# Performance work log

Hardware: AMD Instinct MI355X
Metric: run time of the kernel (lower is better)

The kernel has to match this reference:

```python
import jax, jax.numpy as jnp
import numpy as np

FEATURE_DIM = 128
EDGE_DIM = 32
N_NODES = 10000
BATCH = 4
N_EDGES = 640000
TEMPERATURE = 0.66
POWER_ITERS = 5


def spectral_normalize(W):
    # torch.nn.utils.spectral_norm: divide W by largest singular value estimated
    # via power iteration; u, v are treated as constants (no grad).
    # W: [out, in]
    u = jnp.ones((W.shape[0],), W.dtype) / jnp.sqrt(jnp.asarray(W.shape[0], W.dtype))
    for _ in range(POWER_ITERS):
        v = W.T @ u
        v = v / (jnp.linalg.norm(v) + 1e-12)
        u = W @ v
        u = u / (jnp.linalg.norm(u) + 1e-12)
    u = jax.lax.stop_gradient(u)
    v = jax.lax.stop_gradient(v)
    sigma = u @ (W @ v)
    return W / sigma


def setup_inputs() -> dict:
    key = jax.random.key(0)
    ks = jax.random.split(key, 8)
    node_feat = jax.random.normal(ks[0], (BATCH, N_NODES, FEATURE_DIM), dtype=jnp.float32)
    batch_ids = jax.random.randint(ks[1], (N_EDGES,), 0, BATCH)
    src_nodes = jax.random.randint(ks[2], (N_EDGES,), 0, N_NODES)
    tgt_nodes = jax.random.randint(ks[3], (N_EDGES,), 0, N_NODES)
    in_dim = 2 * FEATURE_DIM + 1  # src_feat ++ tgt_feat ++ distance
    # kaiming_normal_(nonlinearity='relu'): std = sqrt(2 / fan_in)
    W1 = jax.random.normal(ks[4], (EDGE_DIM, in_dim), jnp.float32) * np.sqrt(2.0 / in_dim)
    b1 = jnp.zeros((EDGE_DIM,), jnp.float32)
    W2 = jax.random.normal(ks[5], (EDGE_DIM, EDGE_DIM), jnp.float32) * np.sqrt(2.0 / EDGE_DIM)
    b2 = jnp.zeros((EDGE_DIM,), jnp.float32)
    bound = 0.1 * np.sqrt(6.0 / (EDGE_DIM + 1))
    W3 = jax.random.uniform(ks[6], (1, EDGE_DIM), jnp.float32, -bound, bound)
    b3 = jnp.ones((1,), jnp.float32)
    return {"node_feat": node_feat, "W1": W1, "b1": b1, "W2": W2, "b2": b2,
            "W3": W3, "b3": b3, "batch_ids": batch_ids,
            "src_nodes": src_nodes, "tgt_nodes": tgt_nodes}


def reference(node_feat, W1, b1, W2, b2, W3, b3, batch_ids, src_nodes, tgt_nodes):
    # per-edge gather of endpoint features  [E, D]
    src_feat = node_feat[batch_ids, src_nodes]
    tgt_feat = node_feat[batch_ids, tgt_nodes]
    dist = jnp.linalg.norm(src_feat - tgt_feat, axis=-1, keepdims=True)  # [E,1]
    edge_features = jnp.concatenate([src_feat, tgt_feat, dist], axis=-1)  # [E, 2D+1]
    # spectral-norm MLP (dropout is identity at eval / in this reference)
    h = jax.nn.relu(edge_features @ spectral_normalize(W1).T + b1)
    h = jax.nn.relu(h @ spectral_normalize(W2).T + b2)
    logAlpha = (h @ spectral_normalize(W3).T + b3).squeeze(-1)  # [E]
    logAlpha = jnp.clip(logAlpha, -5.0, 5.0)
    edge_weights = jax.nn.sigmoid(logAlpha / TEMPERATURE)
    return edge_weights, logAlpha
```

## Files before the change

### kernel.cpp

```cpp
#include <hip/hip_runtime.h>
#include <hip/hip_fp16.h>
#include <math.h>

#define FEATD 128
#define NNODES 10000
#define NBATCH 4
#define NROWS (NBATCH*NNODES)

#define OFF_I1   0
#define OFF_W1L  8
#define OFF_W2   64
#define OFF_W3   1088
#define OFF_W2H  1120
#define OFF_P16  4096
#define P16_FLOATS (NROWS*64/2)
#define OFF_FQ   (OFF_P16 + P16_FLOATS)
#define F16_FLOATS (NROWS*FEATD/2)
#define OFF_FBWT OFF_P16

#define WSTRIDE 68
#define PROJ_ROWS 32

typedef _Float16 h2 __attribute__((ext_vector_type(2)));
union U32H2 { unsigned u; h2 h; };
union U4H2  { uint4 u; h2 h[4]; };

#if defined(__has_builtin)
#if __has_builtin(__builtin_amdgcn_fdot2)
#define HAVE_FDOT2 1
#endif
#if __has_builtin(__builtin_amdgcn_cvt_pk_f32_fp8) && __has_builtin(__builtin_amdgcn_cvt_pk_fp8_f32)
#define HAVE_FP8 1
#endif
#endif

__device__ __forceinline__ float fdot2f(h2 a, h2 b, float c) {
#ifdef HAVE_FDOT2
  return __builtin_amdgcn_fdot2(a, b, c, false);
#else
  return c + (float)a[0] * (float)b[0] + (float)a[1] * (float)b[1];
#endif
}

__device__ __forceinline__ float bfly64(float x) {
  x += __shfl_xor(x, 1, 64);
  x += __shfl_xor(x, 2, 64);
  x += __shfl_xor(x, 4, 64);
  x += __shfl_xor(x, 8, 64);
  x += __shfl_xor(x, 16, 64);
  x += __shfl_xor(x, 32, 64);
  return x;
}

#ifdef HAVE_FP8
typedef float floatx2 __attribute__((ext_vector_type(2)));
__device__ __forceinline__ float ssd_fp8_w(unsigned aw, unsigned bw, float s) {
  floatx2 al = __builtin_amdgcn_cvt_pk_f32_fp8((int)aw, false);
  floatx2 ah = __builtin_amdgcn_cvt_pk_f32_fp8((int)aw, true);
  floatx2 bl = __builtin_amdgcn_cvt_pk_f32_fp8((int)bw, false);
  floatx2 bh = __builtin_amdgcn_cvt_pk_f32_fp8((int)bw, true);
  float d0 = al[0] - bl[0], d1 = al[1] - bl[1];
  float d2 = ah[0] - bh[0], d3 = ah[1] - bh[1];
  return s + d0 * d0 + d1 * d1 + d2 * d2 + d3 * d3;
}
__device__ __forceinline__ float grp_dist_fp8(uint2 au, uint2 bu) {
  float ssd = ssd_fp8_w(au.x, bu.x, 0.f);
  ssd = ssd_fp8_w(au.y, bu.y, ssd);
  ssd += __shfl_xor(ssd, 1, 64);
  ssd += __shfl_xor(ssd, 2, 64);
  ssd += __shfl_xor(ssd, 4, 64);
  ssd += __shfl_xor(ssd, 8, 64);
  return sqrtf(ssd);
}
#endif

__global__ __launch_bounds__(64, 1) void spectral64(const float* __restrict__ W1,
                                                    const float* __restrict__ W2,
                                                    const float* __restrict__ W3,
                                                    float* __restrict__ ws) {
  int lane = threadIdx.x;

  float col[4][32];
  float c256[32];
  #pragma unroll
  for (int m = 0; m < 4; ++m)
    #pragma unroll
    for (int j = 0; j < 32; ++j)
      col[m][j] = W1[j * 257 + 64 * m + lane];
  #pragma unroll
  for (int j = 0; j < 32; ++j) c256[j] = W1[j * 257 + 256];

  float u[32];
  #pragma unroll
  for (int j = 0; j < 32; ++j) u[j] = 1.0f;
  float invu = 0.17677669529663687f;
  float nu = 0.f;

  for (int it = 0; it < 5; ++it) {
    float v0 = 0.f, v1 = 0.f, v2 = 0.f, v3 = 0.f, a4 = 0.f;
    #pragma unroll
    for (int j = 0; j < 32; ++j) {
      v0 += col[0][j] * u[j];
      v1 += col[1][j] * u[j];
      v2 += col[2][j] * u[j];
      v3 += col[3][j] * u[j];
      a4 += c256[j] * u[j];
    }
    v0 *= invu; v1 *= invu; v2 *= invu; v3 *= invu;
    float v4 = (lane == 0) ? a4 * invu : 0.f;
    float nv = v0 * v0 + v1 * v1 + v2 * v2 + v3 * v3 + v4 * v4;
    nv = bfly64(nv);
    float invv = 1.0f / (sqrtf(nv) + 1e-12f);

    float b[32];
    #pragma unroll
    for (int j = 0; j < 32; ++j)
      b[j] = (col[0][j] * v0 + col[1][j] * v1 + col[2][j] * v2 +
              col[3][j] * v3 + c256[j] * v4) * invv;
    #pragma unroll
    for (int off = 1; off < 64; off <<= 1) {
      #pragma unroll
      for (int j = 0; j < 32; ++j) b[j] += __shfl_xor(b[j], off, 64);
    }
    nu = 0.f;
    #pragma unroll
    for (int j = 0; j < 32; ++j) { u[j] = b[j]; nu += b[j] * b[j]; }
    invu = 1.0f / (sqrtf(nu) + 1e-12f);
  }
  float sig1 = nu * invu;
  float i1 = 1.0f / sig1;
  if (lane == 0) {
    ws[OFF_I1] = i1;
    #pragma unroll
    for (int j = 0; j < 32; ++j) ws[OFF_W1L + j] = c256[j] * i1;
  }

  float wc[32];
  #pragma unroll
  for (int j = 0; j < 32; ++j)
    wc[j] = (lane < 32) ? W2[j * 32 + (lane & 31)] : 0.f;

  float u2[32];
  #pragma unroll
  for (int j = 0; j < 32; ++j) u2[j] = 1.0f;
  float invu2 = 0.17677669529663687f;
  float nu2 = 0.f;

  for (int it = 0; it < 5; ++it) {
    float a = 0.f;
    #pragma unroll
    for (int j = 0; j < 32; ++j) a += wc[j] * u2[j];
    a *= invu2;
    float nv = bfly64(a * a);
    float invv = 1.0f / (sqrtf(nv) + 1e-12f);
    float b[32];
    #pragma unroll
    for (int j = 0; j < 32; ++j) b[j] = wc[j] * a * invv;
    #pragma unroll
    for (int off = 1; off < 64; off <<= 1) {
      #pragma unroll
      for (int j = 0; j < 32; ++j) b[j] += __shfl_xor(b[j], off, 64);
    }
    nu2 = 0.f;
    #pragma unroll
    for (int j = 0; j < 32; ++j) { u2[j] = b[j]; nu2 += b[j] * b[j]; }
    invu2 = 1.0f / (sqrtf(nu2) + 1e-12f);
  }
  float sig2 = nu2 * invu2;
  float i2 = 1.0f / sig2;

  unsigned* w2h = (unsigned*)(ws + OFF_W2H);
  #pragma unroll
  for (int j = 0; j < 32; ++j) {
    float val = wc[j] * i2;
    float oth = __shfl_xor(val, 1, 64);
    if (lane < 32 && (lane & 1) == 0) {
      U32H2 pk;
      pk.h[0] = (_Float16)val;
      pk.h[1] = (_Float16)oth;
      w2h[j * 16 + (lane >> 1)] = pk.u;
    }
  }

  float w3v = (lane < 32) ? W3[lane & 31] : 0.f;
  float s3 = bfly64(w3v * w3v);
  if (lane < 32) ws[OFF_W3 + lane] = w3v / (sqrtf(s3) + 1e-12f);
}

__global__ __launch_bounds__(256, 3) void proj_kernel(const float* __restrict__ feat,
                                                      const float* __restrict__ W1,
                                                      float* __restrict__ ws,
                                                      int doFQ) {
  __shared__ float sA[128 * WSTRIDE];
  __shared__ float sF[PROJ_ROWS * 128];
  int tid = threadIdx.x;

  for (int idx = tid; idx < 32 * 257; idx += 256) {
    int j = idx / 257, c = idx - j * 257;
    float w = W1[idx];
    if (c < 128) sA[c * WSTRIDE + j] = w;
    else if (c < 256) sA[(c - 128) * WSTRIDE + 32 + j] = w;
  }

  int rbase = blockIdx.x * PROJ_ROWS;
  const float4* Fg = (const float4*)&feat[(size_t)rbase * FEATD];
  char* fq = (char*)(ws + OFF_FQ);
  for (int i = tid; i < PROJ_ROWS * 32; i += 256) {
    float4 f = Fg[i];
    ((float4*)sF)[i] = f;
    if (doFQ) {
#ifdef HAVE_FP8
      unsigned w = __builtin_amdgcn_cvt_pk_fp8_f32(f.x, f.y, 0, false);
      w = __builtin_amdgcn_cvt_pk_fp8_f32(f.z, f.w, (int)w, true);
      *(unsigned*)(fq + (size_t)rbase * 128 + (size_t)i * 4) = w;
#else
      U32H2 a, b; uint2 pk;
      a.h[0] = (_Float16)f.x; a.h[1] = (_Float16)f.y;
      b.h[0] = (_Float16)f.z; b.h[1] = (_Float16)f.w;
      pk.x = a.u; pk.y = b.u;
      *(uint2*)(fq + (size_t)rbase * 256 + (size_t)i * 8) = pk;
#endif
    }
  }
  __syncthreads();

  __half* p16 = (__half*)(ws + OFF_P16);
  int rg = tid >> 4;
  int jg = (tid & 15) << 2;
  int rl0 = rg * 2;
  const float4* F0 = (const float4*)&sF[(rl0 + 0) * 128];
  const float4* F1 = (const float4*)&sF[(rl0 + 1) * 128];
  float acc[2][4] = {{0, 0, 0, 0}, {0, 0, 0, 0}};

  #pragma unroll 4
  for (int k4 = 0; k4 < 32; ++k4) {
    float4 f0 = F0[k4], f1 = F1[k4];
    #pragma unroll
    for (int kk = 0; kk < 4; ++kk) {
      int k = 4 * k4 + kk;
      float4 w = *(const float4*)&sA[k * WSTRIDE + jg];
      float e0 = (kk == 0) ? f0.x : (kk == 1) ? f0.y : (kk == 2) ? f0.z : f0.w;
      float e1 = (kk == 0) ? f1.x : (kk == 1) ? f1.y : (kk == 2) ? f1.z : f1.w;
      acc[0][0] += e0 * w.x; acc[0][1] += e0 * w.y; acc[0][2] += e0 * w.z; acc[0][3] += e0 * w.w;
      acc[1][0] += e1 * w.x; acc[1][1] += e1 * w.y; acc[1][2] += e1 * w.z; acc[1][3] += e1 * w.w;
    }
  }
  #pragma unroll
  for (int r = 0; r < 2; ++r) {
    U32H2 a, b;
    a.h[0] = (_Float16)acc[r][0]; a.h[1] = (_Float16)acc[r][1];
    b.h[0] = (_Float16)acc[r][2]; b.h[1] = (_Float16)acc[r][3];
    uint2 o; o.x = a.u; o.y = b.u;
    *(uint2*)((char*)p16 + (size_t)(rbase + rl0 + r) * 128 + (size_t)jg * 2) = o;
  }
}

__device__ __forceinline__ float grp_dist_f16(uint4 au, uint4 bu) {
  U4H2 a, b; a.u = au; b.u = bu;
  float ssd = 0.f;
  #pragma unroll
  for (int p = 0; p < 4; ++p) { h2 d = a.h[p] - b.h[p]; ssd = fdot2f(d, d, ssd); }
  ssd += __shfl_xor(ssd, 1, 64);
  ssd += __shfl_xor(ssd, 2, 64);
  ssd += __shfl_xor(ssd, 4, 64);
  ssd += __shfl_xor(ssd, 8, 64);
  return sqrtf(ssd);
}

__device__ __forceinline__ unsigned h1pack(unsigned puv, unsigned quv, float dist, float i1,
                                           float w1l0, float w1l1, float bb0, float bb1) {
  U32H2 p, q; p.u = puv; q.u = quv;
  float h0  = fmaxf(fmaf((float)p.h[0] + (float)q.h[0], i1, fmaf(dist, w1l0, bb0)), 0.f);
  float h1v = fmaxf(fmaf((float)p.h[1] + (float)q.h[1], i1, fmaf(dist, w1l1, bb1)), 0.f);
  U32H2 r; r.h[0] = (_Float16)h0; r.h[1] = (_Float16)h1v;
  return r.u;
}

template <bool FQ>
__global__ __launch_bounds__(256, 8) void edge_fused(const float* __restrict__ feat,
                                                     const float* __restrict__ ws,
                                                     const float* __restrict__ b1,
                                                     const float* __restrict__ b2,
                                                     const float* __restrict__ b3,
                                                     const int* __restrict__ bids,
                                                     const int* __restrict__ srcs,
                                                     const int* __restrict__ tgts,
                                                     float* __restrict__ out, int E) {
  __shared__ unsigned ht[256 * 17];
  __shared__ int sRS[256], sRT[256];
  int tid = threadIdx.x;
  int lane = tid & 15;
  int grp  = tid >> 4;

  const char*  featq = (const char*)(ws + OFF_FQ);
  const __half* p16  = (const __half*)(ws + OFF_P16);
  const unsigned* w2h = (const unsigned*)(ws + OFF_W2H);

  float i1 = ws[OFF_I1];
  int j0 = 2 * lane;
  float w1l0 = ws[OFF_W1L + j0];
  float w1l1 = ws[OFF_W1L + j0 + 1];
  float bb0  = b1[j0];
  float bb1  = b1[j0 + 1];
  float bias3 = b3[0];

  for (int base = blockIdx.x * 256; base < E; base += gridDim.x * 256) {
    int e0 = base + tid;
    if (e0 < E) {
      int b = bids[e0];
      sRS[tid] = b * NNODES + srcs[e0];
      sRT[tid] = b * NNODES + tgts[e0];
    }
    __syncthreads();

    if (FQ && (base + 256 <= E)) {
      #pragma unroll 1
      for (int rr = 0; rr < 8; ++rr) {
        int el0 = (rr * 2 + 0) * 16 + grp;
        int el1 = (rr * 2 + 1) * 16 + grp;
        int rs0 = sRS[el0], rt0 = sRT[el0];
        int rs1 = sRS[el1], rt1 = sRT[el1];
#ifdef HAVE_FP8
        uint2 a0 = *(const uint2*)(featq + ((size_t)rs0 << 7) + (lane << 3));
        uint2 c0 = *(const uint2*)(featq + ((size_t)rt0 << 7) + (lane << 3));
        uint2 a1 = *(const uint2*)(featq + ((size_t)rs1 << 7) + (lane << 3));
        uint2 c1 = *(const uint2*)(featq + ((size_t)rt1 << 7) + (lane << 3));
#else
        uint4 a0 = *(const uint4*)(featq + ((size_t)rs0 << 8) + (lane << 4));
        uint4 c0 = *(const uint4*)(featq + ((size_t)rt0 << 8) + (lane << 4));
        uint4 a1 = *(const uint4*)(featq + ((size_t)rs1 << 8) + (lane << 4));
        uint4 c1 = *(const uint4*)(featq + ((size_t)rt1 << 8) + (lane << 4));
#endif
        unsigned pu0 = *(const unsigned*)((const char*)p16 + ((size_t)rs0 << 7) + (lane << 2));
        unsigned qu0 = *(const unsigned*)((const char*)p16 + ((size_t)rt0 << 7) + 64 + (lane << 2));
        unsigned pu1 = *(const unsigned*)((const char*)p16 + ((size_t)rs1 << 7) + (lane << 2));
        unsigned qu1 = *(const unsigned*)((const char*)p16 + ((size_t)rt1 << 7) + 64 + (lane << 2));
#ifdef HAVE_FP8
        float d0 = grp_dist_fp8(a0, c0);
        float d1 = grp_dist_fp8(a1, c1);
#else
        float d0 = grp_dist_f16(a0, c0);
        float d1 = grp_dist_f16(a1, c1);
#endif
        ht[el0 * 17 + lane] = h1pack(pu0, qu0, d0, i1, w1l0, w1l1, bb0, bb1);
        ht[el1 * 17 + lane] = h1pack(pu1, qu1, d1, i1, w1l0, w1l1, bb0, bb1);
      }
    } else {
      #pragma unroll 2
      for (int rr = 0; rr < 16; ++rr) {
        int el = rr * 16 + grp;
        int e  = base + el;
        if (e < E) {
          int rs = sRS[el], rt = sRT[el];
          float dist;
          if (FQ) {
#ifdef HAVE_FP8
            uint2 au = *(const uint2*)(featq + ((size_t)rs << 7) + (lane << 3));
            uint2 bu = *(const uint2*)(featq + ((size_t)rt << 7) + (lane << 3));
            dist = grp_dist_fp8(au, bu);
#else
            uint4 au = *(const uint4*)(featq + ((size_t)rs << 8) + (lane << 4));
            uint4 bu = *(const uint4*)(featq + ((size_t)rt << 8) + (lane << 4));
            dist = grp_dist_f16(au, bu);
#endif
          } else {
            const float4* A  = (const float4*)&feat[(size_t)rs * FEATD];
            const float4* Bp = (const float4*)&feat[(size_t)rt * FEATD];
            float ssd = 0.f;
            #pragma unroll
            for (int p = 0; p < 2; ++p) {
              float4 a = A[lane * 2 + p], c = Bp[lane * 2 + p];
              float dx = a.x - c.x, dy = a.y - c.y, dz = a.z - c.z, dw = a.w - c.w;
              ssd += dx * dx + dy * dy + dz * dz + dw * dw;
            }
            ssd += __shfl_xor(ssd, 1, 64);
            ssd += __shfl_xor(ssd, 2, 64);
            ssd += __shfl_xor(ssd, 4, 64);
            ssd += __shfl_xor(ssd, 8, 64);
            dist = sqrtf(ssd);
          }
          unsigned puv = *(const unsigned*)((const char*)p16 + ((size_t)rs << 7) + (lane << 2));
          unsigned quv = *(const unsigned*)((const char*)p16 + ((size_t)rt << 7) + 64 + (lane << 2));
          ht[el * 17 + lane] = h1pack(puv, quv, dist, i1, w1l0, w1l1, bb0, bb1);
        }
      }
    }
    __syncthreads();

    int e = base + tid;
    if (e < E) {
      unsigned hrow[16];
      #pragma unroll
      for (int q = 0; q < 16; ++q) hrow[q] = ht[tid * 17 + q];
      float la = bias3;
      #pragma unroll
      for (int j = 0; j < 32; ++j) {
        float acc = b2[j];
        #pragma unroll
        for (int q = 0; q < 16; ++q) {
          U32H2 w; w.u = w2h[j * 16 + q];
          U32H2 h; h.u = hrow[q];
          acc = fdot2f(w.h, h.h, acc);
        }
        la += ws[OFF_W3 + j] * fmaxf(acc, 0.f);
      }
      la = fminf(fmaxf(la, -5.f), 5.f);
      out[e]     = 1.0f / (1.0f + exp2f(la * -2.18590179f));
      out[E + e] = la;
    }
    __syncthreads();
  }
}

template <int M, int K>
__device__ float spectral_sigma_t(const float* __restrict__ Wg,
                                  float* sW, float* u, float* v, volatile float* red) {
  int tid = threadIdx.x;
  int wid = tid >> 6, lid = tid & 63;
  int j8 = tid >> 3, l8 = tid & 7;
  for (int i = tid; i < M * K; i += 256) sW[i] = Wg[i];
  if (tid < M) u[tid] = 1.0f;
  __syncthreads();
  float invu = 1.0f / sqrtf((float)M);
  float invv = 0.f;
  for (int it = 0; it < 5; ++it) {
    float p = 0.f;
    for (int k = tid; k < K; k += 256) {
      float a = 0.f;
      #pragma unroll
      for (int j = 0; j < M; ++j) a += sW[j * K + k] * u[j];
      a *= invu;
      v[k] = a;
      p += a * a;
    }
    #pragma unroll
    for (int off = 1; off < 64; off <<= 1) p += __shfl_xor(p, off, 64);
    if (lid == 0) red[wid] = p;
    __syncthreads();
    p = red[0] + red[1] + red[2] + red[3];
    invv = 1.0f / (sqrtf(p) + 1e-12f);
    float a = 0.f;
    if (j8 < M) {
      #pragma unroll
      for (int k = l8; k < K; k += 8) a += sW[j8 * K + k] * v[k];
      a *= invv;
    }
    a += __shfl_xor(a, 1, 64);
    a += __shfl_xor(a, 2, 64);
    a += __shfl_xor(a, 4, 64);
    float q = 0.f;
    if (j8 < M && l8 == 0) { u[j8] = a; q = a * a; }
    #pragma unroll
    for (int off = 1; off < 64; off <<= 1) q += __shfl_xor(q, off, 64);
    if (lid == 0) red[4 + wid] = q;
    __syncthreads();
    q = red[4] + red[5] + red[6] + red[7];
    invu = 1.0f / (sqrtf(q) + 1e-12f);
  }
  float a = 0.f;
  if (j8 < M) {
    #pragma unroll
    for (int k = l8; k < K; k += 8) a += sW[j8 * K + k] * v[k];
  }
  a += __shfl_xor(a, 1, 64);
  a += __shfl_xor(a, 2, 64);
  a += __shfl_xor(a, 4, 64);
  float s = (j8 < M && l8 == 0) ? a * u[j8] : 0.f;
  #pragma unroll
  for (int off = 1; off < 64; off <<= 1) s += __shfl_xor(s, off, 64);
  if (lid == 0) red[wid] = s;
  __syncthreads();
  float sig = (red[0] + red[1] + red[2] + red[3]) * invu * invv;
  __syncthreads();
  return sig;
}

__global__ __launch_bounds__(256) void spectral_full(const float* __restrict__ W1,
                                                     const float* __restrict__ W2,
                                                     const float* __restrict__ W3,
                                                     float* __restrict__ ws) {
  __shared__ float sA[32 * 257];
  __shared__ float u[32], v[257];
  __shared__ float red[8];
  int tid = threadIdx.x;
  float sig1 = spectral_sigma_t<32, 257>(W1, sA, u, v, red);
  float i1 = 1.0f / sig1;
  for (int idx = tid; idx < 128 * 64; idx += 256) {
    int k = idx >> 6, jj = idx & 63;
    float w = (jj < 32) ? sA[jj * 257 + k] : sA[(jj - 32) * 257 + 128 + k];
    ws[OFF_FBWT + idx] = w * i1;
  }
  for (int j = tid; j < 32; j += 256) ws[OFF_W1L + j] = sA[j * 257 + 256] * i1;
  __syncthreads();
  float sig2 = spectral_sigma_t<32, 32>(W2, sA, u, v, red);
  float i2 = 1.0f / sig2;
  for (int idx = tid; idx < 1024; idx += 256) ws[OFF_W2 + idx] = sA[idx] * i2;
  __syncthreads();
  float sig3 = spectral_sigma_t<1, 32>(W3, sA, u, v, red);
  float i3 = 1.0f / sig3;
  for (int k = tid; k < 32; k += 256) ws[OFF_W3 + k] = sA[k] * i3;
}

__global__ __launch_bounds__(256) void edge_kernel_nop(const float* __restrict__ feat,
                                                       const float* __restrict__ ws,
                                                       const float* __restrict__ b1,
                                                       const float* __restrict__ b2,
                                                       const float* __restrict__ b3,
                                                       const int* __restrict__ bids,
                                                       const int* __restrict__ srcs,
                                                       const int* __restrict__ tgts,
                                                       float* __restrict__ out, int E) {
  __shared__ float sWt[128 * 64];
  __shared__ float sW2[1024];
  __shared__ float sW3[32], sW1l[32], sB1[32], sB2[32];
  int tid = threadIdx.x;
  for (int i = tid * 4; i < 128 * 64; i += 256 * 4)
    *(float4*)&sWt[i] = *(const float4*)&ws[OFF_FBWT + i];
  for (int i = tid; i < 1024; i += 256) sW2[i] = ws[OFF_W2 + i];
  if (tid < 32) {
    sW3[tid]  = ws[OFF_W3 + tid];
    sW1l[tid] = ws[OFF_W1L + tid];
    sB1[tid]  = b1[tid];
    sB2[tid]  = b2[tid];
  }
  __syncthreads();
  float bias3 = b3[0];

  for (int e = blockIdx.x * 256 + tid; e < E; e += gridDim.x * 256) {
    int b = bids[e], s = srcs[e], t = tgts[e];
    const float4* A  = (const float4*)&feat[(size_t)(b * NNODES + s) * FEATD];
    const float4* Bp = (const float4*)&feat[(size_t)(b * NNODES + t) * FEATD];
    float ssd = 0.f;
    float h1p[32];
    #pragma unroll
    for (int j = 0; j < 32; ++j) h1p[j] = 0.f;
    #pragma unroll 1
    for (int k4 = 0; k4 < 32; ++k4) {
      float4 a = A[k4], c = Bp[k4];
      float dx = a.x - c.x, dy = a.y - c.y, dz = a.z - c.z, dw = a.w - c.w;
      ssd += dx * dx + dy * dy + dz * dz + dw * dw;
      #pragma unroll
      for (int kk = 0; kk < 4; ++kk) {
        int k = 4 * k4 + kk;
        float fa = (kk == 0) ? a.x : (kk == 1) ? a.y : (kk == 2) ? a.z : a.w;
        float fc = (kk == 0) ? c.x : (kk == 1) ? c.y : (kk == 2) ? c.z : c.w;
        #pragma unroll
        for (int q = 0; q < 8; ++q) {
          float4 w0 = *(const float4*)&sWt[k * 64 + 4 * q];
          float4 w1 = *(const float4*)&sWt[k * 64 + 32 + 4 * q];
          h1p[4*q+0] += fa * w0.x + fc * w1.x;
          h1p[4*q+1] += fa * w0.y + fc * w1.y;
          h1p[4*q+2] += fa * w0.z + fc * w1.z;
          h1p[4*q+3] += fa * w0.w + fc * w1.w;
        }
      }
    }
    float dist = sqrtf(ssd);
    float h1[32];
    #pragma unroll
    for (int j = 0; j < 32; ++j)
      h1[j] = fmaxf(h1p[j] + dist * sW1l[j] + sB1[j], 0.f);
    float la = bias3;
    #pragma unroll
    for (int j = 0; j < 32; ++j) {
      float acc = sB2[j];
      #pragma unroll
      for (int q = 0; q < 8; ++q) {
        float4 w = *(const float4*)&sW2[j * 32 + 4 * q];
        acc += w.x * h1[4 * q] + w.y * h1[4 * q + 1] + w.z * h1[4 * q + 2] + w.w * h1[4 * q + 3];
      }
      la += sW3[j] * fmaxf(acc, 0.f);
    }
    la = fminf(fmaxf(la, -5.f), 5.f);
    out[e]     = 1.0f / (1.0f + __expf(-la / 0.66f));
    out[E + e] = la;
  }
}

extern "C" void kernel_launch(void* const* d_in, const int* in_sizes, int n_in,
                              void* d_out, int out_size, void* d_ws, size_t ws_size,
                              hipStream_t stream) {
  const float* feat = (const float*)d_in[0];
  const float* W1   = (const float*)d_in[1];
  const float* b1   = (const float*)d_in[2];
  const float* W2   = (const float*)d_in[3];
  const float* b2   = (const float*)d_in[4];
  const float* W3   = (const float*)d_in[5];
  const float* b3   = (const float*)d_in[6];
  const int* bids   = (const int*)d_in[7];
  const int* srcs   = (const int*)d_in[8];
  const int* tgts   = (const int*)d_in[9];
  float* out = (float*)d_out;
  float* ws  = (float*)d_ws;
  int E = in_sizes[7];

  size_t need_p  = (size_t)OFF_FQ * sizeof(float);
  size_t need_fq = (size_t)(OFF_FQ + F16_FLOATS) * sizeof(float);
  int egrid = (E + 255) / 256;
  int pgrid = NROWS / PROJ_ROWS;

  if (ws_size >= need_fq) {
    spectral64<<<dim3(1), dim3(64), 0, stream>>>(W1, W2, W3, ws);
    proj_kernel<<<dim3(pgrid), dim3(256), 0, stream>>>(feat, W1, ws, 1);
    edge_fused<true><<<dim3(egrid), dim3(256), 0, stream>>>(feat, ws, b1, b2, b3,
                                                            bids, srcs, tgts, out, E);
  } else if (ws_size >= need_p) {
    spectral64<<<dim3(1), dim3(64), 0, stream>>>(W1, W2, W3, ws);
    proj_kernel<<<dim3(pgrid), dim3(256), 0, stream>>>(feat, W1, ws, 0);
    edge_fused<false><<<dim3(egrid), dim3(256), 0, stream>>>(feat, ws, b1, b2, b3,
                                                             bids, srcs, tgts, out, E);
  } else {
    spectral_full<<<dim3(1), dim3(256), 0, stream>>>(W1, W2, W3, ws);
    edge_kernel_nop<<<dim3(egrid), dim3(256), 0, stream>>>(feat, ws, b1, b2, b3,
                                                           bids, srcs, tgts, out, E);
  }
}
```

Before: 111.2 us.

## Read node features directly from global in projection kernel with 4-row register tiles

```diff
diff --git a/kernel.cpp b/kernel.cpp
--- a/kernel.cpp
+++ b/kernel.cpp
@@ -19,7 +19,6 @@
 #define OFF_FBWT OFF_P16
 
 #define WSTRIDE 68
-#define PROJ_ROWS 32
 
 typedef _Float16 h2 __attribute__((ext_vector_type(2)));
 union U32H2 { unsigned u; h2 h; };
@@ -187,12 +186,11 @@
   if (lane < 32) ws[OFF_W3 + lane] = w3v / (sqrtf(s3) + 1e-12f);
 }
 
-__global__ __launch_bounds__(256, 3) void proj_kernel(const float* __restrict__ feat,
+__global__ __launch_bounds__(256, 4) void proj_kernel(const float* __restrict__ feat,
                                                       const float* __restrict__ W1,
                                                       float* __restrict__ ws,
                                                       int doFQ) {
   __shared__ float sA[128 * WSTRIDE];
-  __shared__ float sF[PROJ_ROWS * 128];
   int tid = threadIdx.x;
 
   for (int idx = tid; idx < 32 * 257; idx += 256) {
@@ -201,57 +199,71 @@
     if (c < 128) sA[c * WSTRIDE + j] = w;
     else if (c < 256) sA[(c - 128) * WSTRIDE + 32 + j] = w;
   }
-
-  int rbase = blockIdx.x * PROJ_ROWS;
-  const float4* Fg = (const float4*)&feat[(size_t)rbase * FEATD];
+  __syncthreads();
+
+  __half* p16 = (__half*)(ws + OFF_P16);
   char* fq = (char*)(ws + OFF_FQ);
-  for (int i = tid; i < PROJ_ROWS * 32; i += 256) {
-    float4 f = Fg[i];
-    ((float4*)sF)[i] = f;
-    if (doFQ) {
+  int rg = tid >> 4;
+  int jg = (tid & 15) << 2;
+  int slice = tid & 15;
+  int r0 = blockIdx.x * 64 + rg * 4;
+  const float4* F0 = (const float4*)&feat[(size_t)(r0 + 0) * FEATD];
+  const float4* F1 = (const float4*)&feat[(size_t)(r0 + 1) * FEATD];
+  const float4* F2 = (const float4*)&feat[(size_t)(r0 + 2) * FEATD];
+  const float4* F3 = (const float4*)&feat[(size_t)(r0 + 3) * FEATD];
+  float acc[4][4] = {{0,0,0,0},{0,0,0,0},{0,0,0,0},{0,0,0,0}};
+
+  #pragma unroll 2
+  for (int k4 = 0; k4 < 32; ++k4) {
+    float4 f0 = F0[k4], f1 = F1[k4], f2 = F2[k4], f3 = F3[k4];
+    if (doFQ && (k4 >> 1) == slice) {
 #ifdef HAVE_FP8
-      unsigned w = __builtin_amdgcn_cvt_pk_fp8_f32(f.x, f.y, 0, false);
-      w = __builtin_amdgcn_cvt_pk_fp8_f32(f.z, f.w, (int)w, true);
-      *(unsigned*)(fq + (size_t)rbase * 128 + (size_t)i * 4) = w;
+      unsigned w;
+      w = __builtin_amdgcn_cvt_pk_fp8_f32(f0.x, f0.y, 0, false);
+      w = __builtin_amdgcn_cvt_pk_fp8_f32(f0.z, f0.w, (int)w, true);
+      *(unsigned*)(fq + (size_t)(r0 + 0) * 128 + (size_t)k4 * 4) = w;
+      w = __builtin_amdgcn_cvt_pk_fp8_f32(f1.x, f1.y, 0, false);
+      w = __builtin_amdgcn_cvt_pk_fp8_f32(f1.z, f1.w, (int)w, true);
+      *(unsigned*)(fq + (size_t)(r0 + 1) * 128 + (size_t)k4 * 4) = w;
+      w = __builtin_amdgcn_cvt_pk_fp8_f32(f2.x, f2.y, 0, false);
+      w = __builtin_amdgcn_cvt_pk_fp8_f32(f2.z, f2.w, (int)w, true);
+      *(unsigned*)(fq + (size_t)(r0 + 2) * 128 + (size_t)k4 * 4) = w;
+      w = __builtin_amdgcn_cvt_pk_fp8_f32(f3.x, f3.y, 0, false);
+      w = __builtin_amdgcn_cvt_pk_fp8_f32(f3.z, f3.w, (int)w, true);
+      *(unsigned*)(fq + (size_t)(r0 + 3) * 128 + (size_t)k4 * 4) = w;
 #else
       U32H2 a, b; uint2 pk;
-      a.h[0] = (_Float16)f.x; a.h[1] = (_Float16)f.y;
-      b.h[0] = (_Float16)f.z; b.h[1] = (_Float16)f.w;
-      pk.x = a.u; pk.y = b.u;
-      *(uint2*)(fq + (size_t)rbase * 256 + (size_t)i * 8) = pk;
-#endif
-    }
-  }
-  __syncthreads();
-
-  __half* p16 = (__half*)(ws + OFF_P16);
-  int rg = tid >> 4;
-  int jg = (tid & 15) << 2;
-  int rl0 = rg * 2;
-  const float4* F0 = (const float4*)&sF[(rl0 + 0) * 128];
-  const float4* F1 = (const float4*)&sF[(rl0 + 1) * 128];
-  float acc[2][4] = {{0, 0, 0, 0}, {0, 0, 0, 0}};
-
-  #pragma unroll 4
-  for (int k4 = 0; k4 < 32; ++k4) {
-    float4 f0 = F0[k4], f1 = F1[k4];
+      a.h[0]=(_Float16)f0.x; a.h[1]=(_Float16)f0.y; b.h[0]=(_Float16)f0.z; b.h[1]=(_Float16)f0.w;
+      pk.x=a.u; pk.y=b.u; *(uint2*)(fq + (size_t)(r0+0)*256 + (size_t)k4*8) = pk;
+      a.h[0]=(_Float16)f1.x; a.h[1]=(_Float16)f1.y; b.h[0]=(_Float16)f1.z; b.h[1]=(_Float16)f1.w;
+      pk.x=a.u; pk.y=b.u; *(uint2*)(fq + (size_t)(r0+1)*256 + (size_t)k4*8) = pk;
+      a.h[0]=(_Float16)f2.x; a.h[1]=(_Float16)f2.y; b.h[0]=(_Float16)f2.z; b.h[1]=(_Float16)f2.w;
+      pk.x=a.u; pk.y=b.u; *(uint2*)(fq + (size_t)(r0+2)*256 + (size_t)k4*8) = pk;
+      a.h[0]=(_Float16)f3.x; a.h[1]=(_Float16)f3.y; b.h[0]=(_Float16)f3.z; b.h[1]=(_Float16)f3.w;
+      pk.x=a.u; pk.y=b.u; *(uint2*)(fq + (size_t)(r0+3)*256 + (size_t)k4*8) = pk;
+#endif
+    }
     #pragma unroll
     for (int kk = 0; kk < 4; ++kk) {
       int k = 4 * k4 + kk;
       float4 w = *(const float4*)&sA[k * WSTRIDE + jg];
       float e0 = (kk == 0) ? f0.x : (kk == 1) ? f0.y : (kk == 2) ? f0.z : f0.w;
       float e1 = (kk == 0) ? f1.x : (kk == 1) ? f1.y : (kk == 2) ? f1.z : f1.w;
+      float e2 = (kk == 0) ? f2.x : (kk == 1) ? f2.y : (kk == 2) ? f2.z : f2.w;
+      float e3 = (kk == 0) ? f3.x : (kk == 1) ? f3.y : (kk == 2) ? f3.z : f3.w;
       acc[0][0] += e0 * w.x; acc[0][1] += e0 * w.y; acc[0][2] += e0 * w.z; acc[0][3] += e0 * w.w;
       acc[1][0] += e1 * w.x; acc[1][1] += e1 * w.y; acc[1][2] += e1 * w.z; acc[1][3] += e1 * w.w;
-    }
-  }
-  #pragma unroll
-  for (int r = 0; r < 2; ++r) {
+      acc[2][0] += e2 * w.x; acc[2][1] += e2 * w.y; acc[2][2] += e2 * w.z; acc[2][3] += e2 * w.w;
+      acc[3][0] += e3 * w.x; acc[3][1] += e3 * w.y; acc[3][2] += e3 * w.z; acc[3][3] += e3 * w.w;
+    }
+  }
+  #pragma unroll
+  for (int r = 0; r < 4; ++r) {
     U32H2 a, b;
     a.h[0] = (_Float16)acc[r][0]; a.h[1] = (_Float16)acc[r][1];
     b.h[0] = (_Float16)acc[r][2]; b.h[1] = (_Float16)acc[r][3];
     uint2 o; o.x = a.u; o.y = b.u;
-    *(uint2*)((char*)p16 + (size_t)(rbase + rl0 + r) * 128 + (size_t)jg * 2) = o;
+    *(uint2*)((char*)p16 + (size_t)(r0 + r) * 128 + (size_t)jg * 2) = o;
   }
 }
 
@@ -597,16 +609,15 @@
   size_t need_p  = (size_t)OFF_FQ * sizeof(float);
   size_t need_fq = (size_t)(OFF_FQ + F16_FLOATS) * sizeof(float);
   int egrid = (E + 255) / 256;
-  int pgrid = NROWS / PROJ_ROWS;
 
   if (ws_size >= need_fq) {
     spectral64<<<dim3(1), dim3(64), 0, stream>>>(W1, W2, W3, ws);
-    proj_kernel<<<dim3(pgrid), dim3(256), 0, stream>>>(feat, W1, ws, 1);
+    proj_kernel<<<dim3(625), dim3(256), 0, stream>>>(feat, W1, ws, 1);
     edge_fused<true><<<dim3(egrid), dim3(256), 0, stream>>>(feat, ws, b1, b2, b3,
                                                             bids, srcs, tgts, out, E);
   } else if (ws_size >= need_p) {
     spectral64<<<dim3(1), dim3(64), 0, stream>>>(W1, W2, W3, ws);
-    proj_kernel<<<dim3(pgrid), dim3(256), 0, stream>>>(feat, W1, ws, 0);
+    proj_kernel<<<dim3(625), dim3(256), 0, stream>>>(feat, W1, ws, 0);
     edge_fused<false><<<dim3(egrid), dim3(256), 0, stream>>>(feat, ws, b1, b2, b3,
                                                              bids, srcs, tgts, out, E);
   } else {
```

Result: slower. 115.0 us (+3.5%).
